# Optimization experiments

Measured on AMD Instinct MI355X. Metric: run time of the kernel, lower is better.

The kernel has to match this reference:

```python
import jax, jax.numpy as jnp
import numpy as np

X_DIM = 20000   # number of input locations (x_l rows)
Y_DIM = 6000    # number of query locations (y_l rows)
REGION_DEG = 10.0  # lon/lat spread so every query has neighbors within 250 km
EARTH_DIAM = 2.0 * 6.378  # thousand-km diameter used by the source
THRESH = 0.25   # 250 km neighborhood threshold


def setup_inputs() -> dict:
    key = jax.random.key(0)
    k1, k2, k3 = jax.random.split(key, 3)
    x = jax.random.normal(k1, (X_DIM, 1), dtype=jnp.float32)
    x_l = jax.random.uniform(k2, (X_DIM, 2), dtype=jnp.float32) * REGION_DEG
    y_l = jax.random.uniform(k3, (Y_DIM, 2), dtype=jnp.float32) * REGION_DEG
    return {"x": x, "x_l": x_l, "y_l": y_l}


def reference(x, x_l, y_l):
    # Training branch of GPR.call, vectorized over the y_dim python loop.
    d2r = jnp.pi / 180.0
    lon_x, lat_x = x_l[:, 0], x_l[:, 1]   # (X,)
    lon_y, lat_y = y_l[:, 0], y_l[:, 1]   # (Y,)
    # haversine terms, shape (Y, X)
    hav = jnp.sin((lat_x[None, :] - lat_y[:, None]) * d2r) ** 2
    hav = hav + (jnp.cos(lat_x * d2r)[None, :] * jnp.cos(lat_y * d2r)[:, None]
                 * jnp.sin((lon_x[None, :] - lon_y[:, None]) * d2r) ** 2)
    d = EARTH_DIAM * jnp.arcsin(jnp.sqrt(hav))  # great-circle distance (thousand km)
    # threshold + gather/scatter in source == masked weights here
    w = jnp.where(d < THRESH, d, 0.0)
    s = jnp.sum(w, axis=1, keepdims=True)        # (Y, 1) per-row normalizer
    L = jnp.where(s > 0, w / jnp.maximum(s, 1e-12), 0.0)  # (Y, X) sparse-ish weights
    m = (L @ x)[:, 0]                            # (Y,) squeezed mean
    # V = 0.001 * I  (noise=None path); returned value is diag_part(V)
    v_diag = jnp.full((y_l.shape[0],), 0.001, dtype=x.dtype)
    return m, v_diag
```

## Files before the change

kernel.cpp:

```cpp
#include <hip/hip_runtime.h>
#include <math.h>


#define TPB    256
#define YPB    4
#define NSTRIP 40
#define NLON   40
#define NCELLS (NSTRIP * NLON)
#define KCAP   64
#define C_CELL   0.25f
#define INV_CELL 4.0f
#define RLAT     1.1250f

__device__ __forceinline__ float sin_poly(float a) {
    float t = a * a;
    return a * fmaf(t, fmaf(t, 8.3333333e-3f, -0.16666667f), 1.0f);
}
__device__ __forceinline__ float cos_poly(float a) {
    float t = a * a;
    return fmaf(t, fmaf(t, fmaf(t, -1.3888889e-3f, 4.1666668e-2f), -0.5f), 1.0f);
}
__device__ __forceinline__ int cell_of(float lon, float lat) {
    int s = (int)(lat * INV_CELL); s = min(max(s, 0), NSTRIP - 1);
    int l = (int)(lon * INV_CELL); l = min(max(l, 0), NLON - 1);
    return s * NLON + l;
}


__global__ __launch_bounds__(TPB) void append_kernel(
    const float* __restrict__ x, const float* __restrict__ x_l,
    int* __restrict__ cnt,
    float4* __restrict__ bA, float2* __restrict__ bRaw,
    float*  __restrict__ bX, int nx)
{
    const float d2r = 0.017453292519943295f;
    int i = blockIdx.x * TPB + threadIdx.x;
    if (i >= nx) return;
    float lon = x_l[2 * i], lat = x_l[2 * i + 1];
    int cell = cell_of(lon, lat);
    int pos = atomicAdd(&cnt[cell], 1);
    if (pos < KCAP) {
        int idx = cell * KCAP + pos;
        float al = lat * d2r, ao = lon * d2r;
        bA[idx]   = make_float4(sin_poly(al), cos_poly(al),
                                sin_poly(ao), cos_poly(ao));
        bRaw[idx] = make_float2(lon, lat);
        bX[idx]   = x[i];
    }
}


__device__ __forceinline__ void point_body(
    const float4* __restrict__ bA, const float2* __restrict__ bRaw,
    const float*  __restrict__ bX, int idx,
    float sly, float cly, float slony, float clony,
    float lon_y, float lat_y, float Hcut,
    float& accw, float& accwx)
{
    const float d2r    = 0.017453292519943295f;
    const float THRESH = 0.25f;
    const float DIAM   = 12.756f;
    const float DIAM6  = 12.756f / 6.0f;
    const float EPS_H  = 5e-8f;

    float4 e  = bA[idx];
    float  xv = bX[idx];

    float sl  = fmaf(e.x, cly,   -(e.y * sly));
    float sd  = fmaf(e.z, clony, -(e.w * slony));
    float cxy = e.y * cly;
    float hav = fmaf(sl, sl, cxy * (sd * sd));

    float tb  = hav - Hcut;
    float r   = __builtin_amdgcn_sqrtf(hav);
    float d   = r * fmaf(hav, DIAM6, DIAM);

    float w;
    if (__builtin_expect(fabsf(tb) < EPS_H, 0)) {
        float2 raw = bRaw[idx];
        float lonx = raw.x, latx = raw.y;

        float dlat = __fsub_rn(latx, lat_y);
        float alat = __fmul_rn(dlat, d2r);
        float slf  = (float)sin((double)alat);
        float h1   = __fmul_rn(slf, slf);

        float axl  = __fmul_rn(latx,  d2r);
        float ayl  = __fmul_rn(lat_y, d2r);
        float cxf  = (float)cos((double)axl);
        float cyf  = (float)cos((double)ayl);
        float cc   = __fmul_rn(cxf, cyf);

        float dlon = __fsub_rn(lonx, lon_y);
        float alon = __fmul_rn(dlon, d2r);
        float sdf  = (float)sin((double)alon);
        float h2   = __fmul_rn(sdf, sdf);

        float hv   = __fadd_rn(h1, __fmul_rn(cc, h2));
        float r32  = (float)sqrt((double)hv);
        float as32 = (float)asin((double)r32);
        float dnp  = __fmul_rn(DIAM, as32);
        w = (dnp < THRESH) ? dnp : 0.0f;
    } else {
        w = (tb < 0.0f) ? d : 0.0f;
    }

    accw += w;
    accwx = fmaf(w, xv, accwx);
}


__global__ __launch_bounds__(TPB) void gpr_bucket(
    const float4* __restrict__ bA, const float2* __restrict__ bRaw,
    const float*  __restrict__ bX, const int* __restrict__ cnt,
    const float*  __restrict__ y_l,
    float* __restrict__ out, int ny, float Hcut, float HcutM)
{
    const int tid  = threadIdx.x;
    const int wave = tid >> 6;
    const int lane = tid & 63;
    const int j    = blockIdx.x * YPB + wave;

    const float d2r = 0.017453292519943295f;
    const float r2d = 57.29577951308232f;

    float lon_y = 0.0f, lat_y = 0.0f;
    if (j < ny) { lon_y = y_l[2 * j]; lat_y = y_l[2 * j + 1]; }

    const float sly   = sin_poly(lat_y * d2r);
    const float cly   = cos_poly(lat_y * d2r);
    const float slony = sin_poly(lon_y * d2r);
    const float clony = cos_poly(lon_y * d2r);

    float accw = 0.0f, accwx = 0.0f;

    const int s0 = max(0,          (int)floorf((lat_y - RLAT) * INV_CELL));
    const int s1 = min(NSTRIP - 1, (int)floorf((lat_y + RLAT) * INV_CELL));

    for (int s = s0; s <= s1; ++s) {
        float slo = s * C_CELL, shi = slo + C_CELL;
        float dmin = fmaxf(0.0f, fmaxf(slo - lat_y, lat_y - shi));
        float de   = fmaxf(0.0f, dmin - 3e-3f);
        float sd_  = sin_poly(de * d2r);
        float rem  = HcutM - sd_ * sd_;
        if (rem <= 0.0f) continue;
        float ccm = cos_poly(fminf(shi, 10.0f) * d2r) * cly * 0.999999f;
        float W   = asinf(fminf(1.0f, sqrtf(rem / ccm))) * r2d + 4e-3f;
        int lo = min(NLON - 1, max(0, (int)floorf((lon_y - W) * INV_CELL)));
        int hi = min(NLON - 1, max(0, (int)floorf((lon_y + W) * INV_CELL)));

        int c = lo;
        while (c <= hi) {
            int cell0 = s * NLON + c;
            int n0 = min(cnt[cell0], KCAP);
            if (c < hi) {
                int n1 = min(cnt[cell0 + 1], KCAP);
                if ((n0 <= 32) & (n1 <= 32)) {
                    int half = lane >> 5;
                    int slot = lane & 31;
                    int cc   = cell0 + half;
                    int nn   = half ? n1 : n0;
                    if (slot < nn)
                        point_body(bA, bRaw, bX, cc * KCAP + slot,
                                   sly, cly, slony, clony,
                                   lon_y, lat_y, Hcut, accw, accwx);
                    c += 2;
                    continue;
                }
            }
            if (lane < n0)
                point_body(bA, bRaw, bX, cell0 * KCAP + lane,
                           sly, cly, slony, clony,
                           lon_y, lat_y, Hcut, accw, accwx);
            c += 1;
        }
    }

    #pragma unroll
    for (int off = 32; off > 0; off >>= 1) {
        accw  += __shfl_xor(accw,  off, 64);
        accwx += __shfl_xor(accwx, off, 64);
    }

    if (lane == 0 && j < ny) {
        float m = (accw > 0.0f) ? (accwx / fmaxf(accw, 1e-12f)) : 0.0f;
        out[j]      = m;
        out[ny + j] = 0.001f;
    }
}


__global__ __launch_bounds__(TPB) void gpr_full(
    const float* __restrict__ x, const float* __restrict__ x_l,
    const float* __restrict__ y_l, float* __restrict__ out,
    int nx, int ny, float Hcut)
{
    __shared__ float4 tA[1024];
    __shared__ float  tX[1024];

    const int tid  = threadIdx.x;
    const int wave = tid >> 6;
    const int lane = tid & 63;
    const int y    = blockIdx.x * YPB + wave;

    const float d2r    = 0.017453292519943295f;
    const float THRESH = 0.25f;
    const float DIAM   = 12.756f;
    const float DIAM6  = 12.756f / 6.0f;
    const float EPS_H  = 5e-8f;

    float lon_y = 0.0f, lat_y = 0.0f;
    if (y < ny) { lon_y = y_l[2 * y]; lat_y = y_l[2 * y + 1]; }
    const float sly   = sin_poly(lat_y * d2r);
    const float cly   = cos_poly(lat_y * d2r);
    const float slony = sin_poly(lon_y * d2r);
    const float clony = cos_poly(lon_y * d2r);

    float accw = 0.0f, accwx = 0.0f;

    const int ntiles = (nx + 1023) / 1024;
    for (int t = 0; t < ntiles; ++t) {
        const int base = t * 1024;
        __syncthreads();
        #pragma unroll
        for (int jj = 0; jj < 1024 / TPB; ++jj) {
            int idx = jj * TPB + tid, i = base + idx;
            if (i < nx) {
                float lon = x_l[2 * i], lat = x_l[2 * i + 1];
                tA[idx] = make_float4(sin_poly(lat * d2r), cos_poly(lat * d2r),
                                      sin_poly(lon * d2r), cos_poly(lon * d2r));
                tX[idx] = x[i];
            }
        }
        __syncthreads();

        const int tn = min(1024, nx - base);
        for (int k = lane; k < tn; k += 64) {
            float4 e  = tA[k];
            float  xv = tX[k];
            float sl  = fmaf(e.x, cly,   -(e.y * sly));
            float sd  = fmaf(e.z, clony, -(e.w * slony));
            float cxy = e.y * cly;
            float hav = fmaf(sl, sl, cxy * (sd * sd));
            float tb  = hav - Hcut;
            float r   = __builtin_amdgcn_sqrtf(hav);
            float d   = r * fmaf(hav, DIAM6, DIAM);
            float w;
            if (__builtin_expect(fabsf(tb) < EPS_H, 0)) {
                int   i    = base + k;
                float lonx = x_l[2 * i], latx = x_l[2 * i + 1];
                float dlat = __fsub_rn(latx, lat_y);
                float alat = __fmul_rn(dlat, d2r);
                float slf  = (float)sin((double)alat);
                float h1   = __fmul_rn(slf, slf);
                float axl  = __fmul_rn(latx,  d2r);
                float ayl  = __fmul_rn(lat_y, d2r);
                float cxf  = (float)cos((double)axl);
                float cyf  = (float)cos((double)ayl);
                float cc   = __fmul_rn(cxf, cyf);
                float dlon = __fsub_rn(lonx, lon_y);
                float alon = __fmul_rn(dlon, d2r);
                float sdf  = (float)sin((double)alon);
                float h2   = __fmul_rn(sdf, sdf);
                float hv   = __fadd_rn(h1, __fmul_rn(cc, h2));
                float r32  = (float)sqrt((double)hv);
                float as32 = (float)asin((double)r32);
                float dnp  = __fmul_rn(DIAM, as32);
                w = (dnp < THRESH) ? dnp : 0.0f;
            } else {
                w = (tb < 0.0f) ? d : 0.0f;
            }
            accw += w;
            accwx = fmaf(w, xv, accwx);
        }
    }

    #pragma unroll
    for (int off = 32; off > 0; off >>= 1) {
        accw  += __shfl_xor(accw,  off, 64);
        accwx += __shfl_xor(accwx, off, 64);
    }

    if (lane == 0 && y < ny) {
        float m = (accw > 0.0f) ? (accwx / fmaxf(accw, 1e-12f)) : 0.0f;
        out[y]      = m;
        out[ny + y] = 0.001f;
    }
}


extern "C" void kernel_launch(void* const* d_in, const int* in_sizes, int n_in,
                              void* d_out, int out_size, void* d_ws, size_t ws_size,
                              hipStream_t stream) {
    const float* x   = (const float*)d_in[0];
    const float* x_l = (const float*)d_in[1];
    const float* y_l = (const float*)d_in[2];
    float* out = (float*)d_out;

    const int nx = in_sizes[0];
    const int ny = in_sizes[2] / 2;

    double th = 0.25 / 12.756;
    double s  = sin(th);
    float Hcut  = (float)(s * s);
    float HcutM = (float)(s * s * 1.001);

    size_t offBA  = 0;
    size_t offBR  = offBA + (size_t)NCELLS * KCAP * sizeof(float4);
    size_t offBX  = offBR + (size_t)NCELLS * KCAP * sizeof(float2);
    size_t offCnt = offBX + (size_t)NCELLS * KCAP * sizeof(float);
    size_t total  = offCnt + (size_t)NCELLS * sizeof(int);

    const int blocks = (ny + YPB - 1) / YPB;

    if (ws_size >= total) {
        float4* bA   = (float4*)((char*)d_ws + offBA);
        float2* bRaw = (float2*)((char*)d_ws + offBR);
        float*  bX   = (float*) ((char*)d_ws + offBX);
        int*    cnt  = (int*)   ((char*)d_ws + offCnt);

        hipMemsetAsync(cnt, 0, (size_t)NCELLS * sizeof(int), stream);
        int nb = (nx + TPB - 1) / TPB;
        append_kernel<<<nb, TPB, 0, stream>>>(x, x_l, cnt, bA, bRaw, bX, nx);
        gpr_bucket<<<blocks, TPB, 0, stream>>>(bA, bRaw, bX, cnt, y_l,
                                               out, ny, Hcut, HcutM);
    } else {
        gpr_full<<<blocks, TPB, 0, stream>>>(x, x_l, y_l, out, nx, ny, Hcut);
    }
}
```

Baseline: 105.8 us.

## Compact per-strip candidate points across wave lanes via prefix-sum and binary search

Replaces the per-cell loop in the query kernel with a per-strip compaction. Each lane loads one cell count, a wave-wide prefix scan computes offsets, and every lane finds its cell by binary search over the shuffled offsets. All 64 lanes then process contiguous candidate points instead of idling on sparse cells. The change also vectorises the coordinate loads into float2. In exchange, each strip pays extra shuffle and scan overhead.

```diff
diff --git a/kernel.cpp b/kernel.cpp
--- a/kernel.cpp
+++ b/kernel.cpp
@@ -36,7 +36,8 @@
     const float d2r = 0.017453292519943295f;
     int i = blockIdx.x * TPB + threadIdx.x;
     if (i >= nx) return;
-    float lon = x_l[2 * i], lat = x_l[2 * i + 1];
+    float2 ll = ((const float2*)x_l)[i];
+    float lon = ll.x, lat = ll.y;
     int cell = cell_of(lon, lat);
     int pos = atomicAdd(&cnt[cell], 1);
     if (pos < KCAP) {
@@ -110,7 +111,7 @@
 }
 
 
-__global__ __launch_bounds__(TPB) void gpr_bucket(
+__global__ __launch_bounds__(TPB) void gpr_compact(
     const float4* __restrict__ bA, const float2* __restrict__ bRaw,
     const float*  __restrict__ bX, const int* __restrict__ cnt,
     const float*  __restrict__ y_l,
@@ -125,7 +126,10 @@
     const float r2d = 57.29577951308232f;
 
     float lon_y = 0.0f, lat_y = 0.0f;
-    if (j < ny) { lon_y = y_l[2 * j]; lat_y = y_l[2 * j + 1]; }
+    if (j < ny) {
+        float2 p = ((const float2*)y_l)[j];
+        lon_y = p.x; lat_y = p.y;
+    }
 
     const float sly   = sin_poly(lat_y * d2r);
     const float cly   = cos_poly(lat_y * d2r);
@@ -138,6 +142,8 @@
     const int s1 = min(NSTRIP - 1, (int)floorf((lat_y + RLAT) * INV_CELL));
 
     for (int s = s0; s <= s1; ++s) {
+        int cr = cnt[s * NLON + min(lane, NLON - 1)];
+
         float slo = s * C_CELL, shi = slo + C_CELL;
         float dmin = fmaxf(0.0f, fmaxf(slo - lat_y, lat_y - shi));
         float de   = fmaxf(0.0f, dmin - 3e-3f);
@@ -149,30 +155,38 @@
         int lo = min(NLON - 1, max(0, (int)floorf((lon_y - W) * INV_CELL)));
         int hi = min(NLON - 1, max(0, (int)floorf((lon_y + W) * INV_CELL)));
 
-        int c = lo;
-        while (c <= hi) {
-            int cell0 = s * NLON + c;
-            int n0 = min(cnt[cell0], KCAP);
-            if (c < hi) {
-                int n1 = min(cnt[cell0 + 1], KCAP);
-                if ((n0 <= 32) & (n1 <= 32)) {
-                    int half = lane >> 5;
-                    int slot = lane & 31;
-                    int cc   = cell0 + half;
-                    int nn   = half ? n1 : n0;
-                    if (slot < nn)
-                        point_body(bA, bRaw, bX, cc * KCAP + slot,
-                                   sly, cly, slony, clony,
-                                   lon_y, lat_y, Hcut, accw, accwx);
-                    c += 2;
-                    continue;
-                }
+        const int ncell = hi - lo + 1;
+        const int cbase = s * NLON + lo;
+
+        int v  = __shfl(cr, min(lo + lane, NLON - 1), 64);
+        int nc = (lane < ncell) ? min(v, KCAP) : 0;
+
+        int pfx = nc;
+        #pragma unroll
+        for (int o = 1; o < 64; o <<= 1) {
+            int t = __shfl_up(pfx, o, 64);
+            if (lane >= o) pfx += t;
+        }
+        const int T   = __shfl(pfx, 63, 64);
+        const int stc = pfx - nc;
+
+        for (int g0 = 0; g0 < T; g0 += 64) {
+            int g  = g0 + lane;
+            int gc = min(g, T - 1);
+
+            int lo_ = 0, hi_ = ncell - 1, sc = 0;
+            #pragma unroll
+            for (int it = 0; it < 6; ++it) {
+                int mid  = (lo_ + hi_ + 1) >> 1;
+                int smid = __shfl(stc, mid, 64);
+                if (smid <= gc) { lo_ = mid; sc = smid; }
+                else            { hi_ = mid - 1; }
             }
-            if (lane < n0)
-                point_body(bA, bRaw, bX, cell0 * KCAP + lane,
+            int idx = (cbase + lo_) * KCAP + (gc - sc);
+            if (g < T)
+                point_body(bA, bRaw, bX, idx,
                            sly, cly, slony, clony,
                            lon_y, lat_y, Hcut, accw, accwx);
-            c += 1;
         }
     }
 
@@ -322,8 +336,8 @@
         hipMemsetAsync(cnt, 0, (size_t)NCELLS * sizeof(int), stream);
         int nb = (nx + TPB - 1) / TPB;
         append_kernel<<<nb, TPB, 0, stream>>>(x, x_l, cnt, bA, bRaw, bX, nx);
-        gpr_bucket<<<blocks, TPB, 0, stream>>>(bA, bRaw, bX, cnt, y_l,
-                                               out, ny, Hcut, HcutM);
+        gpr_compact<<<blocks, TPB, 0, stream>>>(bA, bRaw, bX, cnt, y_l,
+                                                out, ny, Hcut, HcutM);
     } else {
         gpr_full<<<blocks, TPB, 0, stream>>>(x, x_l, y_l, out, nx, ny, Hcut);
     }
```

After: 103.9 us. No clear change (-1.8%).
